# Kernel tuning notes

Hardware: AMD Instinct MI355X
Metric: run time of the kernel (lower is better)

## Reference

```python
import jax, jax.numpy as jnp
import numpy as np

SPARSITY = 0.8  # fraction of weights zeroed (random unstructured mask)

def setup_inputs() -> dict:
    key = jax.random.key(0)
    k1, k2, k3, k4 = jax.random.split(key, 4)
    B, S, D_IN, D_OUT = 4, 2048, 4096, 4096
    x = jax.random.normal(k1, (B, S, D_IN), dtype=jnp.float32)
    weight = jax.random.normal(k2, (D_OUT, D_IN), dtype=jnp.float32) * 0.02
    bias = jax.random.normal(k3, (D_OUT,), dtype=jnp.float32) * 0.02
    # fixed binary mask: keep with prob (1 - sparsity)
    mask = (jax.random.uniform(k4, (D_OUT, D_IN)) >= SPARSITY).astype(jnp.float32)
    return {"x": x, "weight": weight, "bias": bias, "mask": mask}

def reference(x, weight, bias, mask):
    # w = weight * mask; y = x @ w.T + b   (F.linear semantics)
    w = weight * mask                      # [O, I]
    y = jnp.einsum('bsi,oi->bso', x, w)    # [B, S, O]
    return y + bias
```

## Files before the change

kernel.cpp:

```cpp
#include <hip/hip_runtime.h>
#include <hip/hip_bf16.h>
#include <stdint.h>

#define M_DIM 8192
#define N_DIM 4096
#define K_DIM 4096

#define BM 256
#define BN 256
#define BK 64
#define NT (K_DIM / BK)

typedef __attribute__((ext_vector_type(8))) __bf16 bf16x8;
typedef __attribute__((ext_vector_type(4))) float floatx4;

__device__ inline unsigned f2b(float f) {
    union { float f; unsigned u; } v; v.f = f;
    return (v.u + 0x7FFFu + ((v.u >> 16) & 1u)) >> 16;
}
__device__ inline unsigned pk2(float lo, float hi) {
    return (f2b(lo) & 0xFFFFu) | (f2b(hi) << 16);
}

__device__ inline void async_load16(const void* g, void* l) {
    __builtin_amdgcn_global_load_lds(
        (const __attribute__((address_space(1))) unsigned int*)(unsigned long long)g,
        (__attribute__((address_space(3))) unsigned int*)(unsigned int)(unsigned long long)l,
        16, 0, 0);
}

#define SFENCE() asm volatile("" ::: "memory")

__global__ __launch_bounds__(256)
void cvt_x_kernel(const float4* __restrict__ in, uint2* __restrict__ out, int n4) {
    int i = blockIdx.x * blockDim.x + threadIdx.x;
    const int stride = gridDim.x * blockDim.x;
    for (; i < n4; i += stride) {
        float4 a = in[i];
        uint2 o; o.x = pk2(a.x, a.y); o.y = pk2(a.z, a.w);
        out[i] = o;
    }
}

__global__ __launch_bounds__(256)
void cvt_w_kernel(const float4* __restrict__ w, const float4* __restrict__ m,
                  uint2* __restrict__ out, int n4) {
    int i = blockIdx.x * blockDim.x + threadIdx.x;
    const int stride = gridDim.x * blockDim.x;
    for (; i < n4; i += stride) {
        float4 a = w[i], q = m[i];
        uint2 o; o.x = pk2(a.x * q.x, a.y * q.y); o.y = pk2(a.z * q.z, a.w * q.w);
        out[i] = o;
    }
}

__global__ __launch_bounds__(512, 2)
void gemm_8phase(const __hip_bfloat16* __restrict__ A,
                 const __hip_bfloat16* __restrict__ B,
                 const float* __restrict__ bias,
                 float* __restrict__ C) {
    __shared__ __hip_bfloat16 As[2][2][128][64];
    __shared__ __hip_bfloat16 Bs[2][2][128][64];

    const int t    = threadIdx.x;
    const int lane = t & 63;
    const int wave = t >> 6;
    const int wm   = wave >> 2;
    const int wn   = wave & 3;
    const int lm   = lane & 15;
    const int h4   = lane >> 4;

    const int wg = (blockIdx.x & 7) * 64 + (blockIdx.x >> 3);
    const int m0 = (wg >> 4) * BM;
    const int n0 = (wg & 15) * BN;

    const int srow = t >> 3;
    const int schk = t & 7;
    const int sx   = schk ^ (srow & 7);

    const __hip_bfloat16* gA[2][2];
    const __hip_bfloat16* gB[2][2];
#pragma unroll
    for (int h = 0; h < 2; h++)
#pragma unroll
        for (int r = 0; r < 2; r++) {
            gA[h][r] = A + (size_t)(m0 + h * 128 + r * 64 + srow) * K_DIM + sx * 8;
            gB[h][r] = B + (size_t)(n0 + h * 128 + r * 64 + srow) * K_DIM + sx * 8;
        }

#define STAGE_A(b, h, r, tt) \
    async_load16(gA[h][r] + (tt) * BK, &As[b][h][(r) * 64 + srow][schk * 8])
#define STAGE_B(b, h, r, tt) \
    async_load16(gB[h][r] + (tt) * BK, &Bs[b][h][(r) * 64 + srow][schk * 8])

    const int cs0 = ((h4)     ^ (lm & 7)) * 8;
    const int cs1 = ((4 + h4) ^ (lm & 7)) * 8;

#define LDA(b, i, kk) \
    (*(const bf16x8*)&As[b][wm][(i) * 16 + lm][(kk) ? cs1 : cs0])
#define LDB(b, j, kk) \
    (*(const bf16x8*)&Bs[b][wn >> 1][(wn & 1) * 64 + (j) * 16 + lm][(kk) ? cs1 : cs0])

    floatx4 acc[8][4] = {};
    bf16x8 af[4][2], bf01[2][2], bf23[2][2];

    STAGE_A(0, 0, 0, 0); STAGE_A(0, 1, 0, 0);
    STAGE_B(0, 0, 0, 0); STAGE_B(0, 0, 1, 0);
    STAGE_B(0, 1, 0, 0); STAGE_B(0, 1, 1, 0);
    STAGE_A(0, 0, 1, 0); STAGE_A(0, 1, 1, 0);
    STAGE_A(1, 0, 0, 1); STAGE_A(1, 1, 0, 1);
    STAGE_B(1, 0, 0, 1); STAGE_B(1, 0, 1, 1);
    STAGE_B(1, 1, 0, 1); STAGE_B(1, 1, 1, 1);
    asm volatile("s_waitcnt vmcnt(6)" ::: "memory");
    __builtin_amdgcn_s_barrier();
    SFENCE();

    for (int s = 0; s < NT; ++s) {
        const int b  = s & 1;
        const int nb = b ^ 1;

#pragma unroll
        for (int i = 0; i < 4; i++) { af[i][0] = LDA(b, i, 0); af[i][1] = LDA(b, i, 1); }
#pragma unroll
        for (int j = 0; j < 2; j++) { bf01[j][0] = LDB(b, j, 0); bf01[j][1] = LDB(b, j, 1); }
        if (s + 1 < NT) { STAGE_A(nb, 0, 1, s + 1); STAGE_A(nb, 1, 1, s + 1); }
        asm volatile("s_waitcnt lgkmcnt(8)" ::: "memory");
        SFENCE(); __builtin_amdgcn_s_barrier();
        asm volatile("s_waitcnt lgkmcnt(0)" ::: "memory");
        __builtin_amdgcn_s_setprio(1);
#pragma unroll
        for (int i = 0; i < 4; i++)
#pragma unroll
            for (int j = 0; j < 2; j++)
#pragma unroll
                for (int kk = 0; kk < 2; kk++)
                    acc[i][j] = __builtin_amdgcn_mfma_f32_16x16x32_bf16(
                        af[i][kk], bf01[j][kk], acc[i][j], 0, 0, 0);
        __builtin_amdgcn_s_setprio(0);
        SFENCE(); __builtin_amdgcn_s_barrier(); SFENCE();

#pragma unroll
        for (int j = 0; j < 2; j++) { bf23[j][0] = LDB(b, 2 + j, 0); bf23[j][1] = LDB(b, 2 + j, 1); }
        if (s + 2 < NT) { STAGE_A(b, 0, 0, s + 2); STAGE_A(b, 1, 0, s + 2); }
        SFENCE(); __builtin_amdgcn_s_barrier();
        asm volatile("s_waitcnt lgkmcnt(0)" ::: "memory");
        __builtin_amdgcn_s_setprio(1);
#pragma unroll
        for (int i = 0; i < 4; i++)
#pragma unroll
            for (int j = 0; j < 2; j++)
#pragma unroll
                for (int kk = 0; kk < 2; kk++)
                    acc[i][2 + j] = __builtin_amdgcn_mfma_f32_16x16x32_bf16(
                        af[i][kk], bf23[j][kk], acc[i][2 + j], 0, 0, 0);
        __builtin_amdgcn_s_setprio(0);
        SFENCE(); __builtin_amdgcn_s_barrier(); SFENCE();

#pragma unroll
        for (int i = 0; i < 4; i++) { af[i][0] = LDA(b, 4 + i, 0); af[i][1] = LDA(b, 4 + i, 1); }
        if (s + 2 < NT) { STAGE_B(b, 0, 0, s + 2); STAGE_B(b, 0, 1, s + 2); }
        SFENCE(); __builtin_amdgcn_s_barrier();
        asm volatile("s_waitcnt lgkmcnt(0)" ::: "memory");
        __builtin_amdgcn_s_setprio(1);
#pragma unroll
        for (int i = 0; i < 4; i++)
#pragma unroll
            for (int j = 0; j < 2; j++)
#pragma unroll
                for (int kk = 0; kk < 2; kk++)
                    acc[4 + i][j] = __builtin_amdgcn_mfma_f32_16x16x32_bf16(
                        af[i][kk], bf01[j][kk], acc[4 + i][j], 0, 0, 0);
        __builtin_amdgcn_s_setprio(0);
        SFENCE(); __builtin_amdgcn_s_barrier(); SFENCE();

        if (s + 2 < NT) { STAGE_B(b, 1, 0, s + 2); STAGE_B(b, 1, 1, s + 2); }
        __builtin_amdgcn_s_setprio(1);
#pragma unroll
        for (int i = 0; i < 4; i++)
#pragma unroll
            for (int j = 0; j < 2; j++)
#pragma unroll
                for (int kk = 0; kk < 2; kk++)
                    acc[4 + i][2 + j] = __builtin_amdgcn_mfma_f32_16x16x32_bf16(
                        af[i][kk], bf23[j][kk], acc[4 + i][2 + j], 0, 0, 0);
        __builtin_amdgcn_s_setprio(0);
        if (s + 2 < NT) asm volatile("s_waitcnt vmcnt(6)" ::: "memory");
        else            asm volatile("s_waitcnt vmcnt(0)" ::: "memory");
        SFENCE(); __builtin_amdgcn_s_barrier(); SFENCE();
    }

    float bv[4];
#pragma unroll
    for (int j = 0; j < 4; j++)
        bv[j] = bias[n0 + wn * 64 + j * 16 + lm];
    const int row_base = m0 + wm * 128 + h4 * 4;
    const int col_base = n0 + wn * 64 + lm;
#pragma unroll
    for (int i = 0; i < 8; i++)
#pragma unroll
        for (int j = 0; j < 4; j++) {
            const int col = col_base + j * 16;
#pragma unroll
            for (int r = 0; r < 4; r++)
                C[(size_t)(row_base + i * 16 + r) * N_DIM + col] =
                    acc[i][j][r] + bv[j];
        }
}

extern "C" void kernel_launch(void* const* d_in, const int* in_sizes, int n_in,
                              void* d_out, int out_size, void* d_ws, size_t ws_size,
                              hipStream_t stream) {
    const float* x    = (const float*)d_in[0];
    const float* w    = (const float*)d_in[1];
    const float* bias = (const float*)d_in[2];
    const float* mask = (const float*)d_in[3];
    float* out = (float*)d_out;

    __hip_bfloat16* xb = (__hip_bfloat16*)d_ws;
    __hip_bfloat16* wb = xb + (size_t)M_DIM * K_DIM;

    cvt_x_kernel<<<dim3(2048), dim3(256), 0, stream>>>(
        (const float4*)x, (uint2*)xb, M_DIM * K_DIM / 4);
    cvt_w_kernel<<<dim3(2048), dim3(256), 0, stream>>>(
        (const float4*)w, (const float4*)mask, (uint2*)wb, N_DIM * K_DIM / 4);
    gemm_8phase<<<dim3(512), dim3(512), 0, stream>>>(xb, wb, bias, out);
}
```

Baseline: 518.6 us.

## Fuse conversion kernels and restructure GEMM phases by K-half register reuse

The two fp32-to-bf16 conversion kernels become one launch that splits its blocks between x and the masked weight. Each thread now handles 8 elements and writes 16-byte stores. The GEMM main loop is reorganized so each phase loads one K-half of A fragments against all four B column fragments, which keeps B fragments in registers across both M halves. The staging of A and B for step s+2 is regrouped into one phase. This is meant to cut launch overhead and LDS reads per MFMA, at the cost of changed wait counts and the risk of exposing LDS latency in the last phase, which now waits on its own loads.

```diff
diff --git a/kernel.cpp b/kernel.cpp
--- a/kernel.cpp
+++ b/kernel.cpp
@@ -31,26 +31,35 @@
 
 #define SFENCE() asm volatile("" ::: "memory")
 
+#define CVT_GRID 2048
+#define CVT_XBLK 1152
 __global__ __launch_bounds__(256)
-void cvt_x_kernel(const float4* __restrict__ in, uint2* __restrict__ out, int n4) {
-    int i = blockIdx.x * blockDim.x + threadIdx.x;
-    const int stride = gridDim.x * blockDim.x;
-    for (; i < n4; i += stride) {
-        float4 a = in[i];
-        uint2 o; o.x = pk2(a.x, a.y); o.y = pk2(a.z, a.w);
-        out[i] = o;
-    }
-}
-
-__global__ __launch_bounds__(256)
-void cvt_w_kernel(const float4* __restrict__ w, const float4* __restrict__ m,
-                  uint2* __restrict__ out, int n4) {
-    int i = blockIdx.x * blockDim.x + threadIdx.x;
-    const int stride = gridDim.x * blockDim.x;
-    for (; i < n4; i += stride) {
-        float4 a = w[i], q = m[i];
-        uint2 o; o.x = pk2(a.x * q.x, a.y * q.y); o.y = pk2(a.z * q.z, a.w * q.w);
-        out[i] = o;
+void cvt_all(const float4* __restrict__ x, const float4* __restrict__ w,
+             const float4* __restrict__ m, uint4* __restrict__ xb,
+             uint4* __restrict__ wb, int nx8, int nw8) {
+    if ((int)blockIdx.x < CVT_XBLK) {
+        int i = blockIdx.x * 256 + threadIdx.x;
+        const int stride = CVT_XBLK * 256;
+        for (; i < nx8; i += stride) {
+            float4 a = x[2 * i], b = x[2 * i + 1];
+            uint4 o;
+            o.x = pk2(a.x, a.y); o.y = pk2(a.z, a.w);
+            o.z = pk2(b.x, b.y); o.w = pk2(b.z, b.w);
+            xb[i] = o;
+        }
+    } else {
+        int i = ((int)blockIdx.x - CVT_XBLK) * 256 + threadIdx.x;
+        const int stride = (CVT_GRID - CVT_XBLK) * 256;
+        for (; i < nw8; i += stride) {
+            float4 w0 = w[2 * i], w1 = w[2 * i + 1];
+            float4 m0 = m[2 * i], m1 = m[2 * i + 1];
+            uint4 o;
+            o.x = pk2(w0.x * m0.x, w0.y * m0.y);
+            o.y = pk2(w0.z * m0.z, w0.w * m0.w);
+            o.z = pk2(w1.x * m1.x, w1.y * m1.y);
+            o.w = pk2(w1.z * m1.z, w1.w * m1.w);
+            wb[i] = o;
+        }
     }
 }
 
@@ -102,12 +111,12 @@
     (*(const bf16x8*)&Bs[b][wn >> 1][(wn & 1) * 64 + (j) * 16 + lm][(kk) ? cs1 : cs0])
 
     floatx4 acc[8][4] = {};
-    bf16x8 af[4][2], bf01[2][2], bf23[2][2];
+    bf16x8 af[4], bfr[4][2];
 
     STAGE_A(0, 0, 0, 0); STAGE_A(0, 1, 0, 0);
+    STAGE_A(0, 0, 1, 0); STAGE_A(0, 1, 1, 0);
     STAGE_B(0, 0, 0, 0); STAGE_B(0, 0, 1, 0);
     STAGE_B(0, 1, 0, 0); STAGE_B(0, 1, 1, 0);
-    STAGE_A(0, 0, 1, 0); STAGE_A(0, 1, 1, 0);
     STAGE_A(1, 0, 0, 1); STAGE_A(1, 1, 0, 1);
     STAGE_B(1, 0, 0, 1); STAGE_B(1, 0, 1, 1);
     STAGE_B(1, 1, 0, 1); STAGE_B(1, 1, 1, 1);
@@ -120,69 +129,69 @@
         const int nb = b ^ 1;
 
 #pragma unroll
-        for (int i = 0; i < 4; i++) { af[i][0] = LDA(b, i, 0); af[i][1] = LDA(b, i, 1); }
-#pragma unroll
-        for (int j = 0; j < 2; j++) { bf01[j][0] = LDB(b, j, 0); bf01[j][1] = LDB(b, j, 1); }
+        for (int i = 0; i < 4; i++) af[i] = LDA(b, i, 0);
+#pragma unroll
+        for (int j = 0; j < 4; j++) bfr[j][0] = LDB(b, j, 0);
         if (s + 1 < NT) { STAGE_A(nb, 0, 1, s + 1); STAGE_A(nb, 1, 1, s + 1); }
-        asm volatile("s_waitcnt lgkmcnt(8)" ::: "memory");
+        asm volatile("s_waitcnt lgkmcnt(4)" ::: "memory");
         SFENCE(); __builtin_amdgcn_s_barrier();
         asm volatile("s_waitcnt lgkmcnt(0)" ::: "memory");
         __builtin_amdgcn_s_setprio(1);
 #pragma unroll
         for (int i = 0; i < 4; i++)
 #pragma unroll
-            for (int j = 0; j < 2; j++)
-#pragma unroll
-                for (int kk = 0; kk < 2; kk++)
-                    acc[i][j] = __builtin_amdgcn_mfma_f32_16x16x32_bf16(
-                        af[i][kk], bf01[j][kk], acc[i][j], 0, 0, 0);
-        __builtin_amdgcn_s_setprio(0);
-        SFENCE(); __builtin_amdgcn_s_barrier(); SFENCE();
-
-#pragma unroll
-        for (int j = 0; j < 2; j++) { bf23[j][0] = LDB(b, 2 + j, 0); bf23[j][1] = LDB(b, 2 + j, 1); }
-        if (s + 2 < NT) { STAGE_A(b, 0, 0, s + 2); STAGE_A(b, 1, 0, s + 2); }
+            for (int j = 0; j < 4; j++)
+                acc[i][j] = __builtin_amdgcn_mfma_f32_16x16x32_bf16(
+                    af[i], bfr[j][0], acc[i][j], 0, 0, 0);
+        __builtin_amdgcn_s_setprio(0);
+        SFENCE(); __builtin_amdgcn_s_barrier(); SFENCE();
+
+#pragma unroll
+        for (int i = 0; i < 4; i++) af[i] = LDA(b, i, 1);
+#pragma unroll
+        for (int j = 0; j < 4; j++) bfr[j][1] = LDB(b, j, 1);
+        asm volatile("s_waitcnt lgkmcnt(4)" ::: "memory");
         SFENCE(); __builtin_amdgcn_s_barrier();
         asm volatile("s_waitcnt lgkmcnt(0)" ::: "memory");
         __builtin_amdgcn_s_setprio(1);
 #pragma unroll
         for (int i = 0; i < 4; i++)
 #pragma unroll
-            for (int j = 0; j < 2; j++)
-#pragma unroll
-                for (int kk = 0; kk < 2; kk++)
-                    acc[i][2 + j] = __builtin_amdgcn_mfma_f32_16x16x32_bf16(
-                        af[i][kk], bf23[j][kk], acc[i][2 + j], 0, 0, 0);
-        __builtin_amdgcn_s_setprio(0);
-        SFENCE(); __builtin_amdgcn_s_barrier(); SFENCE();
-
-#pragma unroll
-        for (int i = 0; i < 4; i++) { af[i][0] = LDA(b, 4 + i, 0); af[i][1] = LDA(b, 4 + i, 1); }
-        if (s + 2 < NT) { STAGE_B(b, 0, 0, s + 2); STAGE_B(b, 0, 1, s + 2); }
+            for (int j = 0; j < 4; j++)
+                acc[i][j] = __builtin_amdgcn_mfma_f32_16x16x32_bf16(
+                    af[i], bfr[j][1], acc[i][j], 0, 0, 0);
+        __builtin_amdgcn_s_setprio(0);
+        SFENCE(); __builtin_amdgcn_s_barrier(); SFENCE();
+
+#pragma unroll
+        for (int i = 0; i < 4; i++) af[i] = LDA(b, 4 + i, 0);
+        if (s + 2 < NT) {
+            STAGE_A(b, 0, 0, s + 2); STAGE_A(b, 1, 0, s + 2);
+            STAGE_B(b, 0, 0, s + 2); STAGE_B(b, 0, 1, s + 2);
+        }
         SFENCE(); __builtin_amdgcn_s_barrier();
         asm volatile("s_waitcnt lgkmcnt(0)" ::: "memory");
         __builtin_amdgcn_s_setprio(1);
 #pragma unroll
         for (int i = 0; i < 4; i++)
 #pragma unroll
-            for (int j = 0; j < 2; j++)
-#pragma unroll
-                for (int kk = 0; kk < 2; kk++)
-                    acc[4 + i][j] = __builtin_amdgcn_mfma_f32_16x16x32_bf16(
-                        af[i][kk], bf01[j][kk], acc[4 + i][j], 0, 0, 0);
-        __builtin_amdgcn_s_setprio(0);
-        SFENCE(); __builtin_amdgcn_s_barrier(); SFENCE();
-
+            for (int j = 0; j < 4; j++)
+                acc[4 + i][j] = __builtin_amdgcn_mfma_f32_16x16x32_bf16(
+                    af[i], bfr[j][0], acc[4 + i][j], 0, 0, 0);
+        __builtin_amdgcn_s_setprio(0);
+        SFENCE(); __builtin_amdgcn_s_barrier(); SFENCE();
+
+#pragma unroll
+        for (int i = 0; i < 4; i++) af[i] = LDA(b, 4 + i, 1);
         if (s + 2 < NT) { STAGE_B(b, 1, 0, s + 2); STAGE_B(b, 1, 1, s + 2); }
-        __builtin_amdgcn_s_setprio(1);
-#pragma unroll
-        for (int i = 0; i < 4; i++)
-#pragma unroll
-            for (int j = 0; j < 2; j++)
-#pragma unroll
-                for (int kk = 0; kk < 2; kk++)
-                    acc[4 + i][2 + j] = __builtin_amdgcn_mfma_f32_16x16x32_bf16(
-                        af[i][kk], bf23[j][kk], acc[4 + i][2 + j], 0, 0, 0);
+        asm volatile("s_waitcnt lgkmcnt(0)" ::: "memory");
+        __builtin_amdgcn_s_setprio(1);
+#pragma unroll
+        for (int i = 0; i < 4; i++)
+#pragma unroll
+            for (int j = 0; j < 4; j++)
+                acc[4 + i][j] = __builtin_amdgcn_mfma_f32_16x16x32_bf16(
+                    af[i], bfr[j][1], acc[4 + i][j], 0, 0, 0);
         __builtin_amdgcn_s_setprio(0);
         if (s + 2 < NT) asm volatile("s_waitcnt vmcnt(6)" ::: "memory");
         else            asm volatile("s_waitcnt vmcnt(0)" ::: "memory");
@@ -219,9 +228,8 @@
     __hip_bfloat16* xb = (__hip_bfloat16*)d_ws;
     __hip_bfloat16* wb = xb + (size_t)M_DIM * K_DIM;
 
-    cvt_x_kernel<<<dim3(2048), dim3(256), 0, stream>>>(
-        (const float4*)x, (uint2*)xb, M_DIM * K_DIM / 4);
-    cvt_w_kernel<<<dim3(2048), dim3(256), 0, stream>>>(
-        (const float4*)w, (const float4*)mask, (uint2*)wb, N_DIM * K_DIM / 4);
+    cvt_all<<<dim3(CVT_GRID), dim3(256), 0, stream>>>(
+        (const float4*)x, (const float4*)w, (const float4*)mask,
+        (uint4*)xb, (uint4*)wb, M_DIM * K_DIM / 8, N_DIM * K_DIM / 8);
     gemm_8phase<<<dim3(512), dim3(512), 0, stream>>>(xb, wb, bias, out);
 }
```

New measurement: 531.3 us. +2.4%, slower.
